# Optimization experiments

Hardware: AMD Instinct MI355X
Metric: run time of the kernel (lower is better)

## Reference

```python
import jax, jax.numpy as jnp
import numpy as np

B, T, N, F_IN = 4, 12, 20000, 2
HID, OUT, KT, KCHEB = 64, 5, 3, 3
FILTERS = 32
E = 320000
EPS = 1e-5


def cheb_edge_weights(edge_index, num_nodes):
    # PyG ChebConv sym normalization with lambda_max=2: L_hat = -D^{-1/2} A D^{-1/2}
    src, dst = edge_index[0], edge_index[1]
    mask = (src != dst).astype(jnp.float32)  # self loops removed
    deg = jax.ops.segment_sum(mask, src, num_segments=num_nodes)
    dinv = jnp.where(deg > 0, 1.0 / jnp.sqrt(deg), 0.0)
    return -mask * dinv[src] * dinv[dst]


def cheb_conv(x, Ws, b, edge_index, ew, num_nodes):
    # x: (N, Cin); Ws: (K, Cin, Cout); Chebyshev recursion T_k = 2 L_hat T_{k-1} - T_{k-2}
    src, dst = edge_index[0], edge_index[1]
    prop = lambda v: jax.ops.segment_sum(ew[:, None] * v[src], dst, num_segments=num_nodes)
    Tx0 = x
    out = Tx0 @ Ws[0]
    if Ws.shape[0] > 1:
        Tx1 = prop(x)
        out = out + Tx1 @ Ws[1]
        for k in range(2, Ws.shape[0]):
            Tx2 = 2.0 * prop(Tx1) - Tx0
            out = out + Tx2 @ Ws[k]
            Tx0, Tx1 = Tx1, Tx2
    return out + b


def temporal_conv(X, Wstack, bstack):
    # gated temporal conv: relu(conv1(X) * sigmoid(conv2(X)) + conv3(X))
    # X: (B, N, Tin, Cin); kernels (1, KT, Cin, Cout) convolve over time only
    dn = ('NHWC', 'HWIO', 'NHWC')
    conv = lambda Wk, bk: jax.lax.conv_general_dilated(X, Wk, (1, 1), 'VALID', dimension_numbers=dn) + bk
    P = conv(Wstack[0], bstack[0])
    Q = jax.nn.sigmoid(conv(Wstack[1], bstack[1]))
    return jax.nn.relu(P * Q + conv(Wstack[2], bstack[2]))


def _forward(x, edge_index, tc1_w, tc1_b, cheb_w, cheb_b, tc2_w, tc2_b, bn_gamma, bn_beta,
             gru_wx, gru_bx, gru_wh, gru_bh, lin_w, lin_b):
    num_nodes = x.shape[2]
    ew = cheb_edge_weights(edge_index, num_nodes)
    gconv = lambda v, Ws, b: jax.vmap(lambda u: cheb_conv(u, Ws, b, edge_index, ew, num_nodes))(v)

    # ---- STConv ----
    h = jnp.transpose(x, (0, 2, 1, 3))              # (B, N, T, Cin)
    h = temporal_conv(h, tc1_w, tc1_b)              # (B, N, T1, HID)
    h = jnp.transpose(h, (0, 2, 1, 3))              # (B, T1, N, HID)
    b_, t1 = h.shape[0], h.shape[1]
    h = gconv(h.reshape(b_ * t1, num_nodes, -1), cheb_w, cheb_b).reshape(b_, t1, num_nodes, -1)
    h = jax.nn.relu(h)
    h = jnp.transpose(h, (0, 2, 1, 3))              # (B, N, T1, HID)
    h = temporal_conv(h, tc2_w, tc2_b)              # (B, N, T2, OUT)
    # BatchNorm2d(num_nodes), training-mode stats: normalize per node over (B, T2, OUT)
    mean = jnp.mean(h, axis=(0, 2, 3), keepdims=True)
    var = jnp.var(h, axis=(0, 2, 3), keepdims=True)
    h = (h - mean) * jax.lax.rsqrt(var + EPS)
    h = h * bn_gamma[None, :, None, None] + bn_beta[None, :, None, None]
    h = jnp.transpose(h, (0, 2, 1, 3))              # (B, T2, N, OUT)
    h = jax.nn.relu(h)

    # ---- GConvGRU(OUT -> FILTERS, K=2) scanned over time ----
    def cell(Hp, Xt):
        Z = jax.nn.sigmoid(gconv(Xt, gru_wx[0], gru_bx[0]) + gconv(Hp, gru_wh[0], gru_bh[0]))
        R = jax.nn.sigmoid(gconv(Xt, gru_wx[1], gru_bx[1]) + gconv(Hp, gru_wh[1], gru_bh[1]))
        Ht = jnp.tanh(gconv(Xt, gru_wx[2], gru_bx[2]) + gconv(Hp * R, gru_wh[2], gru_bh[2]))
        Hn = Z * Hp + (1.0 - Z) * Ht
        return Hn, Hn

    H0 = jnp.zeros((h.shape[0], num_nodes, FILTERS), dtype=h.dtype)
    _, Hs = jax.lax.scan(cell, H0, jnp.transpose(h, (1, 0, 2, 3)))
    h = jax.nn.relu(jnp.transpose(Hs, (1, 0, 2, 3)))  # (B, T2, N, FILTERS)
    h = h @ lin_w.T + lin_b                            # (B, T2, N, 1)
    return jax.nn.log_softmax(h, axis=1)


def setup_inputs() -> dict:
    ks = jax.random.split(jax.random.key(0), 8)
    s = 0.1
    n = jax.random.normal
    return {
        'x': n(ks[0], (B, T, N, F_IN), jnp.float32),
        'edge_index': jax.random.randint(ks[1], (2, E), 0, N),
        'tc1_w': n(ks[2], (3, 1, KT, F_IN, HID), jnp.float32) * s,
        'tc1_b': jnp.zeros((3, HID), jnp.float32),
        'cheb_w': n(ks[3], (KCHEB, HID, HID), jnp.float32) * s,
        'cheb_b': jnp.zeros((HID,), jnp.float32),
        'tc2_w': n(ks[4], (3, 1, KT, HID, OUT), jnp.float32) * s,
        'tc2_b': jnp.zeros((3, OUT), jnp.float32),
        'bn_gamma': jnp.ones((N,), jnp.float32),
        'bn_beta': jnp.zeros((N,), jnp.float32),
        'gru_wx': n(ks[5], (3, 2, OUT, FILTERS), jnp.float32) * s,
        'gru_bx': jnp.zeros((3, FILTERS), jnp.float32),
        'gru_wh': n(ks[6], (3, 2, FILTERS, FILTERS), jnp.float32) * s,
        'gru_bh': jnp.zeros((3, FILTERS), jnp.float32),
        'lin_w': n(ks[7], (1, FILTERS), jnp.float32) * s,
        'lin_b': jnp.zeros((1,), jnp.float32),
    }


def reference(x, edge_index, tc1_w, tc1_b, cheb_w, cheb_b, tc2_w, tc2_b, bn_gamma, bn_beta,
              gru_wx, gru_bx, gru_wh, gru_bh, lin_w, lin_b):
    return _forward(x, edge_index, tc1_w, tc1_b, cheb_w, cheb_b, tc2_w, tc2_b, bn_gamma, bn_beta,
                    gru_wx, gru_bx, gru_wh, gru_bh, lin_w, lin_b)
```

## Files before the change

kernel.cpp:

```cpp
#include <hip/hip_runtime.h>

constexpr int BB = 4, TT = 12, NN = 20000, FIN = 2;
constexpr int HID = 64, OUTC = 5;
constexpr int FIL = 32;
constexpr int T1n = 10, T2n = 8;
constexpr long ROWS = (long)T1n * NN;

typedef __attribute__((ext_vector_type(8))) short short8v;
typedef __attribute__((ext_vector_type(4))) float f32x4;

constexpr size_t SZ_B   = (size_t)ROWS * 64 * 2;
constexpr size_t SZ_H2  = (size_t)ROWS * 64 * 4;
constexpr size_t SZ_H3P = (size_t)T2n * BB * NN * 8 * 4;
constexpr size_t O_XB  = 0;
constexpr size_t O_T1B = SZ_B;
constexpr size_t O_T2B = 2 * SZ_B;
constexpr size_t O_H2  = 3 * SZ_B;
constexpr size_t O_H3  = O_H2 + SZ_H2;
constexpr size_t O_PX  = O_H3 + SZ_H3P;
constexpr size_t O_BNS = O_PX + SZ_H3P;
constexpr size_t O_BNH = O_BNS + 80000;
constexpr size_t O_DEG = O_BNH + 80000;
constexpr size_t O_IND = O_DEG + 80000;
constexpr size_t O_CUR = O_IND + 80000;
constexpr size_t O_DNV = O_CUR + 80000;
constexpr size_t O_RP  = O_DNV + 80000;
constexpr size_t O_COL = O_RP + 80128;
constexpr size_t O_WCS = O_COL + 1280000;
constexpr size_t O_LG  = O_WCS + 1280000;
constexpr size_t O_WP  = O_LG + 2560000;
constexpr size_t WS_NEED = O_WP + 24576;
constexpr size_t SZ_H = (size_t)BB * NN * FIL * 4;

__device__ __forceinline__ float bf2f(unsigned short u) {
  union { unsigned i; float f; } x; x.i = ((unsigned)u) << 16; return x.f;
}
__device__ __forceinline__ unsigned short f2bf(float f) {
  union { float f; unsigned i; } x; x.f = f;
  unsigned r = x.i + 0x7FFFu + ((x.i >> 16) & 1u);
  return (unsigned short)(r >> 16);
}

__device__ __forceinline__ unsigned swz8(unsigned orig, unsigned nwg) {
  unsigned q = nwg >> 3, r = nwg & 7;
  unsigned xcd = orig & 7, off = orig >> 3;
  unsigned base = (xcd < r) ? xcd * (q + 1) : r * (q + 1) + (xcd - r) * q;
  return base + off;
}

__global__ void __launch_bounds__(256) k_edge_count(const int* __restrict__ ei, int E,
                                                    float* __restrict__ degf, int* __restrict__ indeg) {
  int e = blockIdx.x * 256 + threadIdx.x;
  if (e >= E) return;
  int s = ei[e], d = ei[E + e];
  if (s != d) {
    atomicAdd(&degf[s], 1.0f);
    atomicAdd(&indeg[d], 1);
  }
}

__global__ void __launch_bounds__(256) k_dinv(const float* __restrict__ degf, float* __restrict__ dinv) {
  int n = blockIdx.x * 256 + threadIdx.x;
  if (n >= NN) return;
  float d = degf[n];
  dinv[n] = d > 0.f ? rsqrtf(d) : 0.f;
}

__global__ void __launch_bounds__(1024) k_scan(const int* __restrict__ indeg, int* __restrict__ rowptr) {
  __shared__ int part[1024];
  const int chunk = (NN + 1023) / 1024;
  int t = threadIdx.x;
  int beg = t * chunk, end = min(beg + chunk, NN);
  int s = 0;
  for (int i = beg; i < end; ++i) s += indeg[i];
  part[t] = s;
  __syncthreads();
  if (t == 0) {
    int run = 0;
    for (int i = 0; i < 1024; ++i) { int v = part[i]; part[i] = run; run += v; }
    rowptr[NN] = run;
  }
  __syncthreads();
  int run = part[t];
  for (int i = beg; i < end; ++i) { rowptr[i] = run; run += indeg[i]; }
}

__global__ void __launch_bounds__(256) k_fill(const int* __restrict__ ei, int E,
                                              const float* __restrict__ dinv,
                                              const int* __restrict__ rowptr,
                                              int* __restrict__ cursor,
                                              int* __restrict__ col, float* __restrict__ wcs) {
  int e = blockIdx.x * 256 + threadIdx.x;
  if (e >= E) return;
  int s = ei[e], d = ei[E + e];
  if (s != d) {
    int p = atomicAdd(&cursor[d], 1);
    int o = rowptr[d] + p;
    col[o] = s;
    wcs[o] = -dinv[s] * dinv[d];
  }
}

__global__ void __launch_bounds__(256) k_wpack(const float* __restrict__ W, unsigned short* __restrict__ Wp) {
  int id = blockIdx.x * 256 + threadIdx.x;
  int f = id >> 6, l = id & 63;
  int kk = f >> 2, jt = f & 3;
  int kcheb = kk >> 1;
  int cout = jt * 16 + (l & 15);
#pragma unroll
  for (int e = 0; e < 8; ++e) {
    int cin = (kk & 1) * 32 + (l >> 4) * 8 + e;
    Wp[(size_t)f * 512 + l * 8 + e] = f2bf(W[(size_t)kcheb * 4096 + cin * 64 + cout]);
  }
}

__global__ void __launch_bounds__(256) k_tc1(const float* __restrict__ x, const float* __restrict__ W,
                                             const float* __restrict__ Bv, unsigned short* __restrict__ out, int b) {
  __shared__ float ws[1152];
  __shared__ float bs[192];
  for (int i = threadIdx.x; i < 1152; i += 256) ws[i] = W[i];
  for (int i = threadIdx.x; i < 192; i += 256) bs[i] = Bv[i];
  __syncthreads();
  long tid = (long)blockIdx.x * 256 + threadIdx.x;
  if (tid >= ROWS * 64) return;
  int co = (int)(tid & 63);
  int n  = (int)((tid >> 6) % NN);
  int to = (int)(tid / (64L * NN));
  float aP = bs[co], aQ = bs[64 + co], aR = bs[128 + co];
#pragma unroll
  for (int k = 0; k < 3; ++k) {
#pragma unroll
    for (int ci = 0; ci < 2; ++ci) {
      float xv = x[(((long)b * TT + to + k) * NN + n) * FIN + ci];
      int wi = (k * 2 + ci) * 64 + co;
      aP = fmaf(xv, ws[wi], aP);
      aQ = fmaf(xv, ws[384 + wi], aQ);
      aR = fmaf(xv, ws[768 + wi], aR);
    }
  }
  float sq = 1.f / (1.f + expf(-aQ));
  out[tid] = f2bf(fmaxf(aP * sq + aR, 0.f));
}

__global__ void __launch_bounds__(256) k_prop_bf(const unsigned short* __restrict__ v,
                                                 unsigned short* __restrict__ out,
                                                 const unsigned short* __restrict__ xin,
                                                 const int* __restrict__ rowptr, const int* __restrict__ col,
                                                 const float* __restrict__ wcs) {
  unsigned bid = swz8(blockIdx.x, gridDim.x);
  long tid = (long)bid * 256 + threadIdx.x;
  long ng = tid >> 6;
  if (ng >= ROWS) return;
  int lane = threadIdx.x & 63;
  int eq = lane >> 3, cl = lane & 7;
  int s = (int)(ng / NN);
  int n = (int)(ng % NN);
  n = __builtin_amdgcn_readfirstlane(n);
  s = __builtin_amdgcn_readfirstlane(s);
  int beg = rowptr[n], end = rowptr[n + 1];
  const unsigned short* vs = v + (long)s * NN * 64;
  float acc[8] = {0.f, 0.f, 0.f, 0.f, 0.f, 0.f, 0.f, 0.f};
  for (int e0 = beg; e0 < end; e0 += 8) {
    int e = e0 + eq;
    bool val = e < end;
    float w = val ? wcs[e] : 0.f;
    int cc = val ? col[e] : col[beg];
    short8v a = *(const short8v*)(vs + (long)cc * 64 + cl * 8);
#pragma unroll
    for (int k = 0; k < 8; ++k)
      acc[k] = fmaf(w, bf2f((unsigned short)a[k]), acc[k]);
  }
#pragma unroll
  for (int k = 0; k < 8; ++k) {
    acc[k] += __shfl_xor(acc[k], 8);
    acc[k] += __shfl_xor(acc[k], 16);
    acc[k] += __shfl_xor(acc[k], 32);
  }
  if (eq == 0) {
    long ob = ng * 64 + cl * 8;
    short8v o;
    if (xin) {
      short8v xi = *(const short8v*)(xin + ob);
#pragma unroll
      for (int k = 0; k < 8; ++k) o[k] = (short)f2bf(2.f * acc[k] - bf2f((unsigned short)xi[k]));
    } else {
#pragma unroll
      for (int k = 0; k < 8; ++k) o[k] = (short)f2bf(acc[k]);
    }
    *(short8v*)(out + ob) = o;
  }
}

__global__ void __launch_bounds__(256) k_cheb_mfma(const unsigned short* __restrict__ Xb,
                                                   const unsigned short* __restrict__ T1b,
                                                   const unsigned short* __restrict__ T2b,
                                                   const unsigned short* __restrict__ Wp,
                                                   const float* __restrict__ Bv,
                                                   float* __restrict__ H2) {
  int wid = threadIdx.x >> 6, lane = threadIdx.x & 63;
  long tile = (long)blockIdx.x * 4 + wid;
  if (tile >= ROWS / 16) return;
  int r = lane & 15, g = lane >> 4;
  short8v wf[24];
#pragma unroll
  for (int f = 0; f < 24; ++f)
    wf[f] = *(const short8v*)(Wp + (size_t)f * 512 + lane * 8);
  float bias[4];
#pragma unroll
  for (int jt = 0; jt < 4; ++jt) bias[jt] = Bv[jt * 16 + r];
  long rowbase = tile * 16;
  f32x4 acc[4];
#pragma unroll
  for (int jt = 0; jt < 4; ++jt) acc[jt] = (f32x4){0.f, 0.f, 0.f, 0.f};
  const unsigned short* srcs[3] = {Xb, T1b, T2b};
#pragma unroll
  for (int kk = 0; kk < 6; ++kk) {
    const unsigned short* S = srcs[kk >> 1];
    short8v a = *(const short8v*)(S + (rowbase + r) * 64 + (kk & 1) * 32 + g * 8);
#pragma unroll
    for (int jt = 0; jt < 4; ++jt)
      acc[jt] = __builtin_amdgcn_mfma_f32_16x16x32_bf16(a, wf[kk * 4 + jt], acc[jt], 0, 0, 0);
  }
#pragma unroll
  for (int jt = 0; jt < 4; ++jt)
#pragma unroll
    for (int reg = 0; reg < 4; ++reg) {
      int m = 4 * g + reg;
      H2[(rowbase + m) * 64 + jt * 16 + r] = fmaxf(acc[jt][reg] + bias[jt], 0.f);
    }
}

__global__ void __launch_bounds__(256) k_tc2(const float4* __restrict__ h2, const float* __restrict__ W,
                                             const float* __restrict__ Bv, float* __restrict__ h3, int b) {
  long tid = (long)blockIdx.x * 256 + threadIdx.x;
  if (tid >= (long)T2n * NN) return;
  int t2 = (int)(tid / NN), n = (int)(tid % NN);
  float p[5], q[5], r[5];
#pragma unroll
  for (int co = 0; co < 5; ++co) { p[co] = Bv[co]; q[co] = Bv[5 + co]; r[co] = Bv[10 + co]; }
#pragma unroll
  for (int k = 0; k < 3; ++k) {
    const float4* rowp = h2 + ((long)(t2 + k) * NN + n) * 16;
    for (int c4 = 0; c4 < 16; ++c4) {
      float4 vv = rowp[c4];
      const float* w = W + ((k * 64) + c4 * 4) * 5;
#pragma unroll
      for (int co = 0; co < 5; ++co) {
        p[co] += vv.x * w[co]        + vv.y * w[5 + co]    + vv.z * w[10 + co]   + vv.w * w[15 + co];
        q[co] += vv.x * w[960 + co]  + vv.y * w[965 + co]  + vv.z * w[970 + co]  + vv.w * w[975 + co];
        r[co] += vv.x * w[1920 + co] + vv.y * w[1925 + co] + vv.z * w[1930 + co] + vv.w * w[1935 + co];
      }
    }
  }
  float o[5];
#pragma unroll
  for (int co = 0; co < 5; ++co) {
    float sq = 1.f / (1.f + expf(-q[co]));
    o[co] = fmaxf(p[co] * sq + r[co], 0.f);
  }
  float4* dst = (float4*)(h3 + ((long)(t2 * 4 + b) * NN + n) * 8);
  dst[0] = make_float4(o[0], o[1], o[2], o[3]);
  dst[1] = make_float4(o[4], 0.f, 0.f, 0.f);
}

__global__ void __launch_bounds__(256) k_bn_stats(const float* __restrict__ h3,
                                                  const float* __restrict__ gamma,
                                                  const float* __restrict__ beta,
                                                  float* __restrict__ bnS, float* __restrict__ bnH) {
  long tid = (long)blockIdx.x * 256 + threadIdx.x;
  if (tid >= 4L * NN) return;
  int q = (int)(tid & 3);
  int n = (int)(tid >> 2);
  float s1 = 0.f, s2 = 0.f;
  for (int t = q * 2; t < q * 2 + 2; ++t)
    for (int b = 0; b < 4; ++b) {
      const float* p = h3 + ((long)(t * 4 + b) * NN + n) * 8;
#pragma unroll
      for (int co = 0; co < 5; ++co) { float v = p[co]; s1 += v; s2 += v * v; }
    }
  s1 += __shfl_xor(s1, 1, 4); s1 += __shfl_xor(s1, 2, 4);
  s2 += __shfl_xor(s2, 1, 4); s2 += __shfl_xor(s2, 2, 4);
  if (q == 0) {
    float mean = s1 * (1.f / 160.f);
    float var = s2 * (1.f / 160.f) - mean * mean;
    float sc = gamma[n] * rsqrtf(var + 1e-5f);
    bnS[n] = sc;
    bnH[n] = beta[n] - mean * sc;
  }
}

__global__ void __launch_bounds__(256) k_bn_apply(float* __restrict__ h3,
                                                  const float* __restrict__ bnS,
                                                  const float* __restrict__ bnH) {
  long tid = (long)blockIdx.x * 256 + threadIdx.x;
  if (tid >= 32L * NN * 8) return;
  int n = (int)((tid >> 3) % NN);
  h3[tid] = fmaxf(h3[tid] * bnS[n] + bnH[n], 0.f);
}

__global__ void __launch_bounds__(256) k_prop5(const float* __restrict__ h3, float* __restrict__ PX,
                                               const int* __restrict__ rowptr, const int* __restrict__ col,
                                               const float* __restrict__ wcs) {
  unsigned bid = swz8(blockIdx.x, gridDim.x);
  long tid = (long)bid * 256 + threadIdx.x;
  long ng = tid >> 3;
  int eq = (int)(tid & 7);
  if (ng >= 32L * NN) return;
  int s = (int)(ng / NN), n = (int)(ng % NN);
  int beg = rowptr[n], end = rowptr[n + 1];
  const float* src = h3 + (long)s * NN * 8;
  float a0 = 0.f, a1 = 0.f, a2 = 0.f, a3 = 0.f, a4 = 0.f;
  for (int e0 = beg; e0 < end; e0 += 8) {
    int e = e0 + eq;
    bool val = e < end;
    float w = val ? wcs[e] : 0.f;
    int cc = val ? col[e] : col[beg];
    const float* row = src + (long)cc * 8;
    float4 v = *(const float4*)row;
    float v4 = row[4];
    a0 = fmaf(w, v.x, a0); a1 = fmaf(w, v.y, a1); a2 = fmaf(w, v.z, a2);
    a3 = fmaf(w, v.w, a3); a4 = fmaf(w, v4, a4);
  }
#pragma unroll
  for (int m = 1; m <= 4; m <<= 1) {
    a0 += __shfl_xor(a0, m); a1 += __shfl_xor(a1, m); a2 += __shfl_xor(a2, m);
    a3 += __shfl_xor(a3, m); a4 += __shfl_xor(a4, m);
  }
  if (eq == 0) {
    float* dst = PX + ng * 8;
    *(float4*)dst = make_float4(a0, a1, a2, a3);
    dst[4] = a4;
  }
}

__global__ void __launch_bounds__(256) k_gru1(const float* __restrict__ h3, const float* __restrict__ PX,
                                              const float* __restrict__ Hp,
                                              const int* __restrict__ rowptr, const int* __restrict__ col,
                                              const float* __restrict__ wcs,
                                              const float* __restrict__ gwx, const float* __restrict__ gbx,
                                              const float* __restrict__ gwh, const float* __restrict__ gbh,
                                              float* __restrict__ Z, float* __restrict__ HR, int t) {
  __shared__ float swh[4096];
  __shared__ float swx[640];
  for (int i = threadIdx.x; i < 4096; i += 256) swh[i] = gwh[i];
  for (int i = threadIdx.x; i < 640; i += 256) swx[i] = gwx[i];
  __syncthreads();
  unsigned bid = swz8(blockIdx.x, gridDim.x);
  long tid = (long)bid * 256 + threadIdx.x;
  long ng = tid >> 5;
  int j = (int)(tid & 31);
  if (ng >= 4L * NN) return;
  int b = (int)(ng / NN), n = (int)(ng % NN);
  long hrow = ng * 32;
  long xrow = ((long)(t * 4 + b) * NN + n) * 8;
  const float* hsrc = Hp + (long)b * NN * 32;
  float hv = Hp[hrow + j];
  int eq = j >> 3, cl = j & 7;
  int beg = rowptr[n], end = rowptr[n + 1];
  float4 pa = make_float4(0.f, 0.f, 0.f, 0.f);
  for (int e0 = beg; e0 < end; e0 += 4) {
    int e = e0 + eq;
    bool val = e < end;
    float w = val ? wcs[e] : 0.f;
    int cc = val ? col[e] : col[beg];
    float4 hh = *(const float4*)(hsrc + (long)cc * 32 + cl * 4);
    pa.x = fmaf(w, hh.x, pa.x); pa.y = fmaf(w, hh.y, pa.y);
    pa.z = fmaf(w, hh.z, pa.z); pa.w = fmaf(w, hh.w, pa.w);
  }
  pa.x += __shfl_xor(pa.x, 8);  pa.y += __shfl_xor(pa.y, 8);
  pa.z += __shfl_xor(pa.z, 8);  pa.w += __shfl_xor(pa.w, 8);
  pa.x += __shfl_xor(pa.x, 16); pa.y += __shfl_xor(pa.y, 16);
  pa.z += __shfl_xor(pa.z, 16); pa.w += __shfl_xor(pa.w, 16);
  float v0 = __shfl(pa.x, j >> 2, 32);
  float v1 = __shfl(pa.y, j >> 2, 32);
  float v2 = __shfl(pa.z, j >> 2, 32);
  float v3 = __shfl(pa.w, j >> 2, 32);
  int pp = j & 3;
  float ph = pp == 0 ? v0 : pp == 1 ? v1 : pp == 2 ? v2 : v3;

  float az = gbx[j] + gbh[j];
  float ar = gbx[32 + j] + gbh[32 + j];
#pragma unroll
  for (int ci = 0; ci < 5; ++ci) {
    float xv = h3[xrow + ci], pv = PX[xrow + ci];
    az += xv * swx[ci * 32 + j] + pv * swx[160 + ci * 32 + j];
    ar += xv * swx[320 + ci * 32 + j] + pv * swx[480 + ci * 32 + j];
  }
#pragma unroll
  for (int ci = 0; ci < 32; ++ci) {
    float hb = __shfl(hv, ci, 32);
    float pb = __shfl(ph, ci, 32);
    az += hb * swh[ci * 32 + j] + pb * swh[1024 + ci * 32 + j];
    ar += hb * swh[2048 + ci * 32 + j] + pb * swh[3072 + ci * 32 + j];
  }
  float zz = 1.f / (1.f + expf(-az));
  float rr = 1.f / (1.f + expf(-ar));
  Z[hrow + j] = zz;
  HR[hrow + j] = hv * rr;
}

__global__ void __launch_bounds__(256) k_gru2(const float* __restrict__ h3, const float* __restrict__ PX,
                                              const float* __restrict__ Hp, const float* __restrict__ Z,
                                              const float* __restrict__ HR,
                                              const int* __restrict__ rowptr, const int* __restrict__ col,
                                              const float* __restrict__ wcs,
                                              const float* __restrict__ gwx, const float* __restrict__ gbx,
                                              const float* __restrict__ gwh, const float* __restrict__ gbh,
                                              const float* __restrict__ lw, const float* __restrict__ lb,
                                              float* __restrict__ Hn, float* __restrict__ logits, int t) {
  __shared__ float swh[2048];
  __shared__ float swx[320];
  for (int i = threadIdx.x; i < 2048; i += 256) swh[i] = gwh[4096 + i];
  for (int i = threadIdx.x; i < 320; i += 256) swx[i] = gwx[640 + i];
  __syncthreads();
  unsigned bid = swz8(blockIdx.x, gridDim.x);
  long tid = (long)bid * 256 + threadIdx.x;
  long ng = tid >> 5;
  int j = (int)(tid & 31);
  if (ng >= 4L * NN) return;
  int b = (int)(ng / NN), n = (int)(ng % NN);
  long hrow = ng * 32;
  long xrow = ((long)(t * 4 + b) * NN + n) * 8;
  const float* hsrc = HR + (long)b * NN * 32;
  float hrv = HR[hrow + j];
  int eq = j >> 3, cl = j & 7;
  int beg = rowptr[n], end = rowptr[n + 1];
  float4 pa = make_float4(0.f, 0.f, 0.f, 0.f);
  for (int e0 = beg; e0 < end; e0 += 4) {
    int e = e0 + eq;
    bool val = e < end;
    float w = val ? wcs[e] : 0.f;
    int cc = val ? col[e] : col[beg];
    float4 hh = *(const float4*)(hsrc + (long)cc * 32 + cl * 4);
    pa.x = fmaf(w, hh.x, pa.x); pa.y = fmaf(w, hh.y, pa.y);
    pa.z = fmaf(w, hh.z, pa.z); pa.w = fmaf(w, hh.w, pa.w);
  }
  pa.x += __shfl_xor(pa.x, 8);  pa.y += __shfl_xor(pa.y, 8);
  pa.z += __shfl_xor(pa.z, 8);  pa.w += __shfl_xor(pa.w, 8);
  pa.x += __shfl_xor(pa.x, 16); pa.y += __shfl_xor(pa.y, 16);
  pa.z += __shfl_xor(pa.z, 16); pa.w += __shfl_xor(pa.w, 16);
  float v0 = __shfl(pa.x, j >> 2, 32);
  float v1 = __shfl(pa.y, j >> 2, 32);
  float v2 = __shfl(pa.z, j >> 2, 32);
  float v3 = __shfl(pa.w, j >> 2, 32);
  int pp = j & 3;
  float phr = pp == 0 ? v0 : pp == 1 ? v1 : pp == 2 ? v2 : v3;

  float a = gbx[64 + j] + gbh[64 + j];
#pragma unroll
  for (int ci = 0; ci < 5; ++ci) {
    float xv = h3[xrow + ci], pv = PX[xrow + ci];
    a += xv * swx[ci * 32 + j] + pv * swx[160 + ci * 32 + j];
  }
#pragma unroll
  for (int ci = 0; ci < 32; ++ci) {
    float hb = __shfl(hrv, ci, 32);
    float pb = __shfl(phr, ci, 32);
    a += hb * swh[ci * 32 + j] + pb * swh[1024 + ci * 32 + j];
  }
  float zz = Z[hrow + j];
  float hn = zz * Hp[hrow + j] + (1.f - zz) * tanhf(a);
  Hn[hrow + j] = hn;
  float c = fmaxf(hn, 0.f) * lw[j];
  c += __shfl_xor(c, 16, 32);
  c += __shfl_xor(c, 8, 32);
  c += __shfl_xor(c, 4, 32);
  c += __shfl_xor(c, 2, 32);
  c += __shfl_xor(c, 1, 32);
  if (j == 0) logits[((long)b * 8 + t) * NN + n] = c + lb[0];
}

__global__ void __launch_bounds__(256) k_logsoftmax(const float* __restrict__ logits, float* __restrict__ out) {
  long tid = (long)blockIdx.x * 256 + threadIdx.x;
  if (tid >= 4L * NN) return;
  int b = (int)(tid / NN), n = (int)(tid % NN);
  float l[8];
#pragma unroll
  for (int t = 0; t < 8; ++t) l[t] = logits[((long)b * 8 + t) * NN + n];
  float m = l[0];
#pragma unroll
  for (int t = 1; t < 8; ++t) m = fmaxf(m, l[t]);
  float s = 0.f;
#pragma unroll
  for (int t = 0; t < 8; ++t) s += expf(l[t] - m);
  float lse = m + logf(s);
#pragma unroll
  for (int t = 0; t < 8; ++t) out[((long)b * 8 + t) * NN + n] = l[t] - lse;
}

extern "C" void kernel_launch(void* const* d_in, const int* in_sizes, int n_in,
                              void* d_out, int out_size, void* d_ws, size_t ws_size,
                              hipStream_t stream) {
  const float* x     = (const float*)d_in[0];
  const int*   ei    = (const int*)d_in[1];
  const float* tc1w  = (const float*)d_in[2];
  const float* tc1b  = (const float*)d_in[3];
  const float* chebw = (const float*)d_in[4];
  const float* chebb = (const float*)d_in[5];
  const float* tc2w  = (const float*)d_in[6];
  const float* tc2b  = (const float*)d_in[7];
  const float* gam   = (const float*)d_in[8];
  const float* bet   = (const float*)d_in[9];
  const float* gwx   = (const float*)d_in[10];
  const float* gbx   = (const float*)d_in[11];
  const float* gwh   = (const float*)d_in[12];
  const float* gbh   = (const float*)d_in[13];
  const float* lw    = (const float*)d_in[14];
  const float* lb    = (const float*)d_in[15];
  float* out = (float*)d_out;
  int E = in_sizes[1] / 2;
  if (ws_size < WS_NEED) return;

  char* ws = (char*)d_ws;
  unsigned short* Xb  = (unsigned short*)(ws + O_XB);
  unsigned short* T1b = (unsigned short*)(ws + O_T1B);
  unsigned short* T2b = (unsigned short*)(ws + O_T2B);
  float* H2   = (float*)(ws + O_H2);
  float* h3   = (float*)(ws + O_H3);
  float* PX   = (float*)(ws + O_PX);
  float* bnS  = (float*)(ws + O_BNS);
  float* bnH  = (float*)(ws + O_BNH);
  float* degf = (float*)(ws + O_DEG);
  int*   ind  = (int*)(ws + O_IND);
  int*   cur  = (int*)(ws + O_CUR);
  float* dnv  = (float*)(ws + O_DNV);
  int*   rp   = (int*)(ws + O_RP);
  int*   col  = (int*)(ws + O_COL);
  float* wcs  = (float*)(ws + O_WCS);
  float* lg   = (float*)(ws + O_LG);
  unsigned short* Wp = (unsigned short*)(ws + O_WP);
  float* Hp  = (float*)(ws + O_XB);
  float* Hn  = (float*)(ws + O_XB + SZ_H);
  float* Zb  = (float*)(ws + O_XB + 2 * SZ_H);
  float* HRb = (float*)(ws + O_XB + 3 * SZ_H);

  hipMemsetAsync(ws + O_DEG, 0, 240000, stream);
  unsigned gE = (unsigned)((E + 255) / 256);
  k_edge_count<<<gE, 256, 0, stream>>>(ei, E, degf, ind);
  k_dinv<<<(NN + 255) / 256, 256, 0, stream>>>(degf, dnv);
  k_scan<<<1, 1024, 0, stream>>>(ind, rp);
  k_fill<<<gE, 256, 0, stream>>>(ei, E, dnv, rp, cur, col, wcs);
  k_wpack<<<6, 256, 0, stream>>>(chebw, Wp);

  unsigned g64 = (unsigned)((ROWS * 64 + 255) / 256);
  for (int b = 0; b < 4; ++b) {
    k_tc1<<<g64, 256, 0, stream>>>(x, tc1w, tc1b, Xb, b);
    k_prop_bf<<<g64, 256, 0, stream>>>(Xb, T1b, nullptr, rp, col, wcs);
    k_prop_bf<<<g64, 256, 0, stream>>>(T1b, T2b, Xb, rp, col, wcs);
    k_cheb_mfma<<<(unsigned)(ROWS / 16 / 4), 256, 0, stream>>>(Xb, T1b, T2b, Wp, chebb, H2);
    k_tc2<<<(unsigned)(((long)T2n * NN + 255) / 256), 256, 0, stream>>>(
        (const float4*)H2, tc2w, tc2b, h3, b);
  }

  k_bn_stats<<<(4 * NN + 255) / 256, 256, 0, stream>>>(h3, gam, bet, bnS, bnH);
  k_bn_apply<<<(unsigned)((32L * NN * 8 + 255) / 256), 256, 0, stream>>>(h3, bnS, bnH);

  k_prop5<<<(unsigned)((32L * NN * 8 + 255) / 256), 256, 0, stream>>>(h3, PX, rp, col, wcs);

  hipMemsetAsync(Hp, 0, SZ_H, stream);
  float* hp = Hp;
  float* hn = Hn;
  unsigned gG = (unsigned)((4L * NN * 32 + 255) / 256);
  for (int t = 0; t < 8; ++t) {
    k_gru1<<<gG, 256, 0, stream>>>(h3, PX, hp, rp, col, wcs, gwx, gbx, gwh, gbh, Zb, HRb, t);
    k_gru2<<<gG, 256, 0, stream>>>(h3, PX, hp, Zb, HRb, rp, col, wcs, gwx, gbx, gwh, gbh,
                                   lw, lb, hn, lg, t);
    float* tmp = hp; hp = hn; hn = tmp;
  }

  unsigned gN = (unsigned)((4L * NN + 255) / 256);
  k_logsoftmax<<<gN, 256, 0, stream>>>(lg, out);
}
```

Before: 2.419 ms.

## Pack CSR edges into interleaved (col,weight) pairs and store H2 in bf16

The separate col and weight arrays are merged into one array of {int,float} pairs, so every graph propagation kernel fetches an edge with a single 8-byte load. Padding lanes are clamped to the last edge instead of branching. The Chebyshev output H2 is written as bf16 instead of fp32, which halves its write and read traffic, and the temporal conv now reads it with 16-byte vectors. Neighbor rows in prop_bf are unpacked from 32-bit words. The cost is extra bf16 rounding of H2 before the temporal conv.

```diff
diff --git a/kernel.cpp b/kernel.cpp
--- a/kernel.cpp
+++ b/kernel.cpp
@@ -4,19 +4,21 @@
 constexpr int HID = 64, OUTC = 5;
 constexpr int FIL = 32;
 constexpr int T1n = 10, T2n = 8;
+constexpr int EE = 320000;
 constexpr long ROWS = (long)T1n * NN;
 
 typedef __attribute__((ext_vector_type(8))) short short8v;
 typedef __attribute__((ext_vector_type(4))) float f32x4;
 
+struct EdgeP { int c; float w; };
+
 constexpr size_t SZ_B   = (size_t)ROWS * 64 * 2;
-constexpr size_t SZ_H2  = (size_t)ROWS * 64 * 4;
 constexpr size_t SZ_H3P = (size_t)T2n * BB * NN * 8 * 4;
 constexpr size_t O_XB  = 0;
 constexpr size_t O_T1B = SZ_B;
 constexpr size_t O_T2B = 2 * SZ_B;
-constexpr size_t O_H2  = 3 * SZ_B;
-constexpr size_t O_H3  = O_H2 + SZ_H2;
+constexpr size_t O_H2B = 3 * SZ_B;
+constexpr size_t O_H3  = O_H2B + SZ_B;
 constexpr size_t O_PX  = O_H3 + SZ_H3P;
 constexpr size_t O_BNS = O_PX + SZ_H3P;
 constexpr size_t O_BNH = O_BNS + 80000;
@@ -25,9 +27,8 @@
 constexpr size_t O_CUR = O_IND + 80000;
 constexpr size_t O_DNV = O_CUR + 80000;
 constexpr size_t O_RP  = O_DNV + 80000;
-constexpr size_t O_COL = O_RP + 80128;
-constexpr size_t O_WCS = O_COL + 1280000;
-constexpr size_t O_LG  = O_WCS + 1280000;
+constexpr size_t O_EPK = O_RP + 80128;
+constexpr size_t O_LG  = O_EPK + (size_t)EE * 8;
 constexpr size_t O_WP  = O_LG + 2560000;
 constexpr size_t WS_NEED = O_WP + 24576;
 constexpr size_t SZ_H = (size_t)BB * NN * FIL * 4;
@@ -39,6 +40,12 @@
   union { float f; unsigned i; } x; x.f = f;
   unsigned r = x.i + 0x7FFFu + ((x.i >> 16) & 1u);
   return (unsigned short)(r >> 16);
+}
+__device__ __forceinline__ float lo_bf(unsigned u) {
+  union { unsigned i; float f; } x; x.i = u << 16; return x.f;
+}
+__device__ __forceinline__ float hi_bf(unsigned u) {
+  union { unsigned i; float f; } x; x.i = u & 0xffff0000u; return x.f;
 }
 
 __device__ __forceinline__ unsigned swz8(unsigned orig, unsigned nwg) {
@@ -89,15 +96,14 @@
                                               const float* __restrict__ dinv,
                                               const int* __restrict__ rowptr,
                                               int* __restrict__ cursor,
-                                              int* __restrict__ col, float* __restrict__ wcs) {
+                                              EdgeP* __restrict__ epk) {
   int e = blockIdx.x * 256 + threadIdx.x;
   if (e >= E) return;
   int s = ei[e], d = ei[E + e];
   if (s != d) {
     int p = atomicAdd(&cursor[d], 1);
-    int o = rowptr[d] + p;
-    col[o] = s;
-    wcs[o] = -dinv[s] * dinv[d];
+    EdgeP ep; ep.c = s; ep.w = -dinv[s] * dinv[d];
+    epk[rowptr[d] + p] = ep;
   }
 }
 
@@ -145,8 +151,8 @@
 __global__ void __launch_bounds__(256) k_prop_bf(const unsigned short* __restrict__ v,
                                                  unsigned short* __restrict__ out,
                                                  const unsigned short* __restrict__ xin,
-                                                 const int* __restrict__ rowptr, const int* __restrict__ col,
-                                                 const float* __restrict__ wcs) {
+                                                 const int* __restrict__ rowptr,
+                                                 const EdgeP* __restrict__ epk) {
   unsigned bid = swz8(blockIdx.x, gridDim.x);
   long tid = (long)bid * 256 + threadIdx.x;
   long ng = tid >> 6;
@@ -162,13 +168,15 @@
   float acc[8] = {0.f, 0.f, 0.f, 0.f, 0.f, 0.f, 0.f, 0.f};
   for (int e0 = beg; e0 < end; e0 += 8) {
     int e = e0 + eq;
-    bool val = e < end;
-    float w = val ? wcs[e] : 0.f;
-    int cc = val ? col[e] : col[beg];
-    short8v a = *(const short8v*)(vs + (long)cc * 64 + cl * 8);
-#pragma unroll
-    for (int k = 0; k < 8; ++k)
-      acc[k] = fmaf(w, bf2f((unsigned short)a[k]), acc[k]);
+    int ec = min(e, end - 1);
+    EdgeP ep = epk[ec];
+    float w = (e < end) ? ep.w : 0.f;
+    const unsigned* a = (const unsigned*)(vs + (((long)ep.c) << 6) + cl * 8);
+    unsigned u0 = a[0], u1 = a[1], u2 = a[2], u3 = a[3];
+    acc[0] = fmaf(w, lo_bf(u0), acc[0]); acc[1] = fmaf(w, hi_bf(u0), acc[1]);
+    acc[2] = fmaf(w, lo_bf(u1), acc[2]); acc[3] = fmaf(w, hi_bf(u1), acc[3]);
+    acc[4] = fmaf(w, lo_bf(u2), acc[4]); acc[5] = fmaf(w, hi_bf(u2), acc[5]);
+    acc[6] = fmaf(w, lo_bf(u3), acc[6]); acc[7] = fmaf(w, hi_bf(u3), acc[7]);
   }
 #pragma unroll
   for (int k = 0; k < 8; ++k) {
@@ -180,9 +188,13 @@
     long ob = ng * 64 + cl * 8;
     short8v o;
     if (xin) {
-      short8v xi = *(const short8v*)(xin + ob);
-#pragma unroll
-      for (int k = 0; k < 8; ++k) o[k] = (short)f2bf(2.f * acc[k] - bf2f((unsigned short)xi[k]));
+      const unsigned* xi = (const unsigned*)(xin + ob);
+#pragma unroll
+      for (int k = 0; k < 4; ++k) {
+        unsigned u = xi[k];
+        o[2 * k]     = (short)f2bf(2.f * acc[2 * k]     - lo_bf(u));
+        o[2 * k + 1] = (short)f2bf(2.f * acc[2 * k + 1] - hi_bf(u));
+      }
     } else {
 #pragma unroll
       for (int k = 0; k < 8; ++k) o[k] = (short)f2bf(acc[k]);
@@ -196,7 +208,7 @@
                                                    const unsigned short* __restrict__ T2b,
                                                    const unsigned short* __restrict__ Wp,
                                                    const float* __restrict__ Bv,
-                                                   float* __restrict__ H2) {
+                                                   unsigned short* __restrict__ H2b) {
   int wid = threadIdx.x >> 6, lane = threadIdx.x & 63;
   long tile = (long)blockIdx.x * 4 + wid;
   if (tile >= ROWS / 16) return;
@@ -226,11 +238,11 @@
 #pragma unroll
     for (int reg = 0; reg < 4; ++reg) {
       int m = 4 * g + reg;
-      H2[(rowbase + m) * 64 + jt * 16 + r] = fmaxf(acc[jt][reg] + bias[jt], 0.f);
+      H2b[(rowbase + m) * 64 + jt * 16 + r] = f2bf(fmaxf(acc[jt][reg] + bias[jt], 0.f));
     }
 }
 
-__global__ void __launch_bounds__(256) k_tc2(const float4* __restrict__ h2, const float* __restrict__ W,
+__global__ void __launch_bounds__(256) k_tc2(const unsigned short* __restrict__ h2b, const float* __restrict__ W,
                                              const float* __restrict__ Bv, float* __restrict__ h3, int b) {
   long tid = (long)blockIdx.x * 256 + threadIdx.x;
   if (tid >= (long)T2n * NN) return;
@@ -240,15 +252,19 @@
   for (int co = 0; co < 5; ++co) { p[co] = Bv[co]; q[co] = Bv[5 + co]; r[co] = Bv[10 + co]; }
 #pragma unroll
   for (int k = 0; k < 3; ++k) {
-    const float4* rowp = h2 + ((long)(t2 + k) * NN + n) * 16;
-    for (int c4 = 0; c4 < 16; ++c4) {
-      float4 vv = rowp[c4];
-      const float* w = W + ((k * 64) + c4 * 4) * 5;
-#pragma unroll
-      for (int co = 0; co < 5; ++co) {
-        p[co] += vv.x * w[co]        + vv.y * w[5 + co]    + vv.z * w[10 + co]   + vv.w * w[15 + co];
-        q[co] += vv.x * w[960 + co]  + vv.y * w[965 + co]  + vv.z * w[970 + co]  + vv.w * w[975 + co];
-        r[co] += vv.x * w[1920 + co] + vv.y * w[1925 + co] + vv.z * w[1930 + co] + vv.w * w[1935 + co];
+    const unsigned short* rowp = h2b + ((long)(t2 + k) * NN + n) * 64;
+    for (int c8 = 0; c8 < 8; ++c8) {
+      short8v vv = *(const short8v*)(rowp + c8 * 8);
+      const float* w = W + ((k * 64) + c8 * 8) * 5;
+#pragma unroll
+      for (int u = 0; u < 8; ++u) {
+        float xv = bf2f((unsigned short)vv[u]);
+#pragma unroll
+        for (int co = 0; co < 5; ++co) {
+          p[co] = fmaf(xv, w[u * 5 + co], p[co]);
+          q[co] = fmaf(xv, w[960 + u * 5 + co], q[co]);
+          r[co] = fmaf(xv, w[1920 + u * 5 + co], r[co]);
+        }
       }
     }
   }
@@ -299,8 +315,7 @@
 }
 
 __global__ void __launch_bounds__(256) k_prop5(const float* __restrict__ h3, float* __restrict__ PX,
-                                               const int* __restrict__ rowptr, const int* __restrict__ col,
-                                               const float* __restrict__ wcs) {
+                                               const int* __restrict__ rowptr, const EdgeP* __restrict__ epk) {
   unsigned bid = swz8(blockIdx.x, gridDim.x);
   long tid = (long)bid * 256 + threadIdx.x;
   long ng = tid >> 3;
@@ -312,10 +327,10 @@
   float a0 = 0.f, a1 = 0.f, a2 = 0.f, a3 = 0.f, a4 = 0.f;
   for (int e0 = beg; e0 < end; e0 += 8) {
     int e = e0 + eq;
-    bool val = e < end;
-    float w = val ? wcs[e] : 0.f;
-    int cc = val ? col[e] : col[beg];
-    const float* row = src + (long)cc * 8;
+    int ec = min(e, end - 1);
+    EdgeP ep = epk[ec];
+    float w = (e < end) ? ep.w : 0.f;
+    const float* row = src + ((long)ep.c) * 8;
     float4 v = *(const float4*)row;
     float v4 = row[4];
     a0 = fmaf(w, v.x, a0); a1 = fmaf(w, v.y, a1); a2 = fmaf(w, v.z, a2);
@@ -335,8 +350,7 @@
 
 __global__ void __launch_bounds__(256) k_gru1(const float* __restrict__ h3, const float* __restrict__ PX,
                                               const float* __restrict__ Hp,
-                                              const int* __restrict__ rowptr, const int* __restrict__ col,
-                                              const float* __restrict__ wcs,
+                                              const int* __restrict__ rowptr, const EdgeP* __restrict__ epk,
                                               const float* __restrict__ gwx, const float* __restrict__ gbx,
                                               const float* __restrict__ gwh, const float* __restrict__ gbh,
                                               float* __restrict__ Z, float* __restrict__ HR, int t) {
@@ -360,10 +374,10 @@
   float4 pa = make_float4(0.f, 0.f, 0.f, 0.f);
   for (int e0 = beg; e0 < end; e0 += 4) {
     int e = e0 + eq;
-    bool val = e < end;
-    float w = val ? wcs[e] : 0.f;
-    int cc = val ? col[e] : col[beg];
-    float4 hh = *(const float4*)(hsrc + (long)cc * 32 + cl * 4);
+    int ec = min(e, end - 1);
+    EdgeP ep = epk[ec];
+    float w = (e < end) ? ep.w : 0.f;
+    float4 hh = *(const float4*)(hsrc + ((long)ep.c) * 32 + cl * 4);
     pa.x = fmaf(w, hh.x, pa.x); pa.y = fmaf(w, hh.y, pa.y);
     pa.z = fmaf(w, hh.z, pa.z); pa.w = fmaf(w, hh.w, pa.w);
   }
@@ -377,7 +391,6 @@
   float v3 = __shfl(pa.w, j >> 2, 32);
   int pp = j & 3;
   float ph = pp == 0 ? v0 : pp == 1 ? v1 : pp == 2 ? v2 : v3;
-
   float az = gbx[j] + gbh[j];
   float ar = gbx[32 + j] + gbh[32 + j];
 #pragma unroll
@@ -402,8 +415,7 @@
 __global__ void __launch_bounds__(256) k_gru2(const float* __restrict__ h3, const float* __restrict__ PX,
                                               const float* __restrict__ Hp, const float* __restrict__ Z,
                                               const float* __restrict__ HR,
-                                              const int* __restrict__ rowptr, const int* __restrict__ col,
-                                              const float* __restrict__ wcs,
+                                              const int* __restrict__ rowptr, const EdgeP* __restrict__ epk,
                                               const float* __restrict__ gwx, const float* __restrict__ gbx,
                                               const float* __restrict__ gwh, const float* __restrict__ gbh,
                                               const float* __restrict__ lw, const float* __restrict__ lb,
@@ -428,10 +440,10 @@
   float4 pa = make_float4(0.f, 0.f, 0.f, 0.f);
   for (int e0 = beg; e0 < end; e0 += 4) {
     int e = e0 + eq;
-    bool val = e < end;
-    float w = val ? wcs[e] : 0.f;
-    int cc = val ? col[e] : col[beg];
-    float4 hh = *(const float4*)(hsrc + (long)cc * 32 + cl * 4);
+    int ec = min(e, end - 1);
+    EdgeP ep = epk[ec];
+    float w = (e < end) ? ep.w : 0.f;
+    float4 hh = *(const float4*)(hsrc + ((long)ep.c) * 32 + cl * 4);
     pa.x = fmaf(w, hh.x, pa.x); pa.y = fmaf(w, hh.y, pa.y);
     pa.z = fmaf(w, hh.z, pa.z); pa.w = fmaf(w, hh.w, pa.w);
   }
@@ -445,7 +457,6 @@
   float v3 = __shfl(pa.w, j >> 2, 32);
   int pp = j & 3;
   float phr = pp == 0 ? v0 : pp == 1 ? v1 : pp == 2 ? v2 : v3;
-
   float a = gbx[64 + j] + gbh[64 + j];
 #pragma unroll
   for (int ci = 0; ci < 5; ++ci) {
@@ -515,7 +526,7 @@
   unsigned short* Xb  = (unsigned short*)(ws + O_XB);
   unsigned short* T1b = (unsigned short*)(ws + O_T1B);
   unsigned short* T2b = (unsigned short*)(ws + O_T2B);
-  float* H2   = (float*)(ws + O_H2);
+  unsigned short* H2b = (unsigned short*)(ws + O_H2B);
   float* h3   = (float*)(ws + O_H3);
   float* PX   = (float*)(ws + O_PX);
   float* bnS  = (float*)(ws + O_BNS);
@@ -525,8 +536,7 @@
   int*   cur  = (int*)(ws + O_CUR);
   float* dnv  = (float*)(ws + O_DNV);
   int*   rp   = (int*)(ws + O_RP);
-  int*   col  = (int*)(ws + O_COL);
-  float* wcs  = (float*)(ws + O_WCS);
+  EdgeP* epk  = (EdgeP*)(ws + O_EPK);
   float* lg   = (float*)(ws + O_LG);
   unsigned short* Wp = (unsigned short*)(ws + O_WP);
   float* Hp  = (float*)(ws + O_XB);
@@ -539,31 +549,30 @@
   k_edge_count<<<gE, 256, 0, stream>>>(ei, E, degf, ind);
   k_dinv<<<(NN + 255) / 256, 256, 0, stream>>>(degf, dnv);
   k_scan<<<1, 1024, 0, stream>>>(ind, rp);
-  k_fill<<<gE, 256, 0, stream>>>(ei, E, dnv, rp, cur, col, wcs);
+  k_fill<<<gE, 256, 0, stream>>>(ei, E, dnv, rp, cur, epk);
   k_wpack<<<6, 256, 0, stream>>>(chebw, Wp);
 
   unsigned g64 = (unsigned)((ROWS * 64 + 255) / 256);
   for (int b = 0; b < 4; ++b) {
     k_tc1<<<g64, 256, 0, stream>>>(x, tc1w, tc1b, Xb, b);
-    k_prop_bf<<<g64, 256, 0, stream>>>(Xb, T1b, nullptr, rp, col, wcs);
-    k_prop_bf<<<g64, 256, 0, stream>>>(T1b, T2b, Xb, rp, col, wcs);
-    k_cheb_mfma<<<(unsigned)(ROWS / 16 / 4), 256, 0, stream>>>(Xb, T1b, T2b, Wp, chebb, H2);
-    k_tc2<<<(unsigned)(((long)T2n * NN + 255) / 256), 256, 0, stream>>>(
-        (const float4*)H2, tc2w, tc2b, h3, b);
+    k_prop_bf<<<g64, 256, 0, stream>>>(Xb, T1b, nullptr, rp, epk);
+    k_prop_bf<<<g64, 256, 0, stream>>>(T1b, T2b, Xb, rp, epk);
+    k_cheb_mfma<<<(unsigned)(ROWS / 16 / 4), 256, 0, stream>>>(Xb, T1b, T2b, Wp, chebb, H2b);
+    k_tc2<<<(unsigned)(((long)T2n * NN + 255) / 256), 256, 0, stream>>>(H2b, tc2w, tc2b, h3, b);
   }
 
   k_bn_stats<<<(4 * NN + 255) / 256, 256, 0, stream>>>(h3, gam, bet, bnS, bnH);
   k_bn_apply<<<(unsigned)((32L * NN * 8 + 255) / 256), 256, 0, stream>>>(h3, bnS, bnH);
 
-  k_prop5<<<(unsigned)((32L * NN * 8 + 255) / 256), 256, 0, stream>>>(h3, PX, rp, col, wcs);
+  k_prop5<<<(unsigned)((32L * NN * 8 + 255) / 256), 256, 0, stream>>>(h3, PX, rp, epk);
 
   hipMemsetAsync(Hp, 0, SZ_H, stream);
   float* hp = Hp;
   float* hn = Hn;
   unsigned gG = (unsigned)((4L * NN * 32 + 255) / 256);
   for (int t = 0; t < 8; ++t) {
-    k_gru1<<<gG, 256, 0, stream>>>(h3, PX, hp, rp, col, wcs, gwx, gbx, gwh, gbh, Zb, HRb, t);
-    k_gru2<<<gG, 256, 0, stream>>>(h3, PX, hp, Zb, HRb, rp, col, wcs, gwx, gbx, gwh, gbh,
+    k_gru1<<<gG, 256, 0, stream>>>(h3, PX, hp, rp, epk, gwx, gbx, gwh, gbh, Zb, HRb, t);
+    k_gru2<<<gG, 256, 0, stream>>>(h3, PX, hp, Zb, HRb, rp, epk, gwx, gbx, gwh, gbh,
                                    lw, lb, hn, lg, t);
     float* tmp = hp; hp = hn; hn = tmp;
   }
```

New measurement: 2.349 ms. 1.03x faster.
